# Kernel tuning notes

Measured on AMD Instinct MI355X. Metric: run time of the kernel, lower is better.

Reference implementation:

```python
import jax, jax.numpy as jnp
import numpy as np

USER = 1000
CATE = 1400
FEAT = 128
B = 8192


def setup_inputs() -> dict:
    key = jax.random.key(0)
    ks = jax.random.split(key, 16)
    s = 0.05
    return {
        "feat": jax.random.normal(ks[0], (B, FEAT), jnp.float32),
        "fcat": jax.random.randint(ks[1], (B, 3), 0, CATE),
        "fusr": jax.random.randint(ks[2], (B,), 0, USER),
        "fitm": jax.random.randint(ks[3], (B,), 0, USER),
        "flg": 1,
        "usr_w": jax.random.normal(ks[4], (USER, 128), jnp.float32) * s,
        "cate_w": jax.random.normal(ks[5], (CATE, 11), jnp.float32) * s,
        "cmat_w": jax.random.normal(ks[6], (CATE, 11 * 11), jnp.float32) * s,
        "cbias_w": jax.random.normal(ks[7], (CATE, 11), jnp.float32) * s,
        "ubias_w": jax.random.normal(ks[8], (USER, 128), jnp.float32) * s,
        "cbiasb_w": jax.random.normal(ks[9], (CATE, 95), jnp.float32) * s,
        "fc0_w": jax.random.normal(ks[10], (95, FEAT), jnp.float32) * s,
        "fc0_b": jax.random.normal(ks[11], (95,), jnp.float32) * s,
        "cvismat_w": jax.random.normal(ks[12], (CATE, 95 * 95), jnp.float32) * s,
        "cvisbias_w": jax.random.normal(ks[13], (CATE, 95), jnp.float32) * s,
    }


def reference(feat, fcat, fusr, fitm, flg, usr_w, cate_w, cmat_w, cbias_w,
              ubias_w, cbiasb_w, fc0_w, fc0_b, cvismat_w, cvisbias_w):
    b = feat.shape[0]
    c0, c1, c2 = fcat[:, 0], fcat[:, 1], fcat[:, 2]
    # cat1.repeat(1,11)*cmat .view(b,11,11).sum(2) == batched matvec M @ v
    cat1 = cate_w[c0]                                              # [b,11]
    cat2 = jnp.einsum('bij,bj->bi', cmat_w[c1].reshape(b, 11, 11), cat1) + cbias_w[c1]
    cat3 = jnp.einsum('bij,bj->bi', cmat_w[c2].reshape(b, 11, 11), cat2) + cbias_w[c2]
    cbias = jnp.concatenate([jnp.zeros((b, 33), feat.dtype), cbiasb_w[c2]], axis=1)  # [b,128]
    p0 = feat @ fc0_w.T + fc0_b                                    # [b,95]
    itmq = jnp.einsum('bij,bj->bi', cvismat_w[c2].reshape(b, 95, 95), p0) + cvisbias_w[c2]
    pitm = jnp.concatenate([cat1, cat2, cat3, itmq], axis=1)       # [b,128]
    if flg == 0:
        return jnp.sum((pitm + ubias_w[fusr]) * (usr_w[fusr] + cbias), axis=1).reshape(-1, 1)
    # flg != 0: score against all USER users; algebraic expansion avoids [b,USER,128]
    # sum_d (pitm[b,d]+ubias[u,d])*(usr[u,d]+cbias[b,d])
    return (pitm @ usr_w.T
            + jnp.sum(pitm * cbias, axis=1, keepdims=True)
            + jnp.sum(ubias_w * usr_w, axis=1)[None, :]
            + cbias @ ubias_w.T)                                    # [b,USER]
```

## Files before the change

### kernel.cpp

```cpp
#include <hip/hip_runtime.h>
#include <hip/hip_bf16.h>

typedef unsigned short u16;
typedef unsigned int u32;
typedef u16 u16x4 __attribute__((ext_vector_type(4)));
typedef u16 u16x8 __attribute__((ext_vector_type(8)));
typedef __bf16 bf16x8 __attribute__((ext_vector_type(8)));
typedef float f32x4 __attribute__((ext_vector_type(4)));

#define USER_N 1000
#define CATE_N 1400
#define FEAT_N 128
#define B_N 8192
#define CAP 64

__device__ __forceinline__ float b2f(u16 u) {
    union { u32 i; float f; } v; v.i = ((u32)u) << 16; return v.f;
}
__device__ __forceinline__ u16 f2b(float f) {
    union { float f; u32 i; } v; v.f = f;
    u32 x = v.i;
    u32 r = (x + 0x7fffu + ((x >> 16) & 1u)) >> 16;
    return (u16)r;
}
__device__ __forceinline__ f32x4 ld4u(const float* p) {
    f32x4 v; __builtin_memcpy(&v, p, 16); return v;
}
__device__ __forceinline__ bf16x8 cvt8(f32x4 a, f32x4 b) {
    u16x8 r = {f2b(a.x), f2b(a.y), f2b(a.z), f2b(a.w),
               f2b(b.x), f2b(b.y), f2b(b.z), f2b(b.w)};
    return __builtin_bit_cast(bf16x8, r);
}
__device__ __forceinline__ size_t xa_addr(int b, int k) {
    return (size_t)(b >> 4) * 4096 + (size_t)(k >> 3) * 128 + (b & 15) * 8 + (k & 7);
}

__global__ __launch_bounds__(256) void pack_kernel(
    const float* __restrict__ usr_w, const float* __restrict__ ubias_w,
    const float* __restrict__ feat, const float* __restrict__ fc0_w,
    u16* __restrict__ WB, float* __restrict__ t, int* __restrict__ counts,
    u16* __restrict__ FA, u16* __restrict__ WF)
{
    const int bx = blockIdx.x;
    const int tid = threadIdx.x;
    if (bx < 128) {
        if (bx == 0) {
            for (int i = tid; i < CATE_N; i += 256) counts[i] = 0;
        }
        const int gid = bx * 256 + tid;
        const int u = gid >> 5;
        const int l = gid & 31;
        float part = 0.f;
        u16x4 wa = {0, 0, 0, 0}, wb = {0, 0, 0, 0};
        if (u < USER_N) {
            f32x4 a4 = *(const f32x4*)&usr_w[u * 128 + l * 4];
            f32x4 b4 = *(const f32x4*)&ubias_w[u * 128 + l * 4];
            wa = (u16x4){f2b(a4.x), f2b(a4.y), f2b(a4.z), f2b(a4.w)};
            wb = (u16x4){f2b(b4.x), f2b(b4.y), f2b(b4.z), f2b(b4.w)};
            part = a4.x * b4.x + a4.y * b4.y + a4.z * b4.z + a4.w * b4.w;
        }
        const int nb = u >> 4, lm = u & 15;
        const int ks = l >> 3, quad = (l >> 1) & 3, j0 = (l & 1) * 4;
        *(u16x4*)&WB[(size_t)(nb * 8 + ks) * 512 + quad * 128 + lm * 8 + j0] = wa;
        *(u16x4*)&WB[(size_t)(nb * 8 + 4 + ks) * 512 + quad * 128 + lm * 8 + j0] = wb;
        part += __shfl_xor(part, 16, 32);
        part += __shfl_xor(part, 8, 32);
        part += __shfl_xor(part, 4, 32);
        part += __shfl_xor(part, 2, 32);
        part += __shfl_xor(part, 1, 32);
        if (l == 0) t[u] = part;
    } else if (bx < 256) {
        const int lm = tid >> 4;
        const int q4 = tid & 15;
        const int ks = q4 >> 2, quad = q4 & 3;
        #pragma unroll
        for (int it = 0; it < 4; ++it) {
            const int mt = (bx - 128) * 4 + it;
            const float* fr = feat + (size_t)(mt * 16 + lm) * 128 + ks * 32 + quad * 8;
            f32x4 lo = *(const f32x4*)fr;
            f32x4 hi = *(const f32x4*)(fr + 4);
            *(u16x8*)&FA[(size_t)mt * 2048 + ks * 512 + quad * 128 + lm * 8] =
                __builtin_bit_cast(u16x8, cvt8(lo, hi));
        }
    } else {
        const int lm = tid & 15;
        const int quad = (tid >> 4) & 3;
        const int ks = tid >> 6;
        #pragma unroll
        for (int nt = 0; nt < 6; ++nt) {
            const int i = nt * 16 + lm;
            const bool v = (i < 95);
            f32x4 lo = {0, 0, 0, 0}, hi = {0, 0, 0, 0};
            if (v) {
                const float* br = fc0_w + (size_t)i * 128 + ks * 32 + quad * 8;
                lo = *(const f32x4*)br;
                hi = *(const f32x4*)(br + 4);
            }
            *(u16x8*)&WF[(size_t)(nt * 4 + ks) * 512 + quad * 128 + lm * 8] =
                __builtin_bit_cast(u16x8, cvt8(lo, hi));
        }
    }
}

__global__ __launch_bounds__(256) void p0chain_kernel(
    const int* __restrict__ fcat,
    const float* __restrict__ cate_w, const float* __restrict__ cmat_w,
    const float* __restrict__ cbias_w, const float* __restrict__ fc0_b,
    const u16* __restrict__ FA, const u16* __restrict__ WF,
    int* __restrict__ counts, int* __restrict__ bins,
    u16* __restrict__ p0Gb, u16* __restrict__ XA)
{
    const int tid = threadIdx.x;
    const int w = tid >> 6, lane = tid & 63;
    const int lm = lane & 15, quad = lane >> 4;
    const int b0 = blockIdx.x * 32;

    if (tid < 32) {
        int row = b0 + tid;
        int c2v = fcat[row * 3 + 2];
        int slot = atomicAdd(&counts[c2v], 1);
        if (slot < CAP) bins[c2v * CAP + slot] = row;
    }

    const int mt = blockIdx.x * 2 + (w >> 1);
    const int nth = w & 1;
    bf16x8 a[4];
    const u16* fa = FA + (size_t)mt * 2048 + quad * 128 + lm * 8;
    #pragma unroll
    for (int ks = 0; ks < 4; ++ks)
        a[ks] = __builtin_bit_cast(bf16x8, *(const u16x8*)(fa + ks * 512));

    #pragma unroll
    for (int nt3 = 0; nt3 < 3; ++nt3) {
        const int nt = nth * 3 + nt3;
        const u16* wf = WF + (size_t)(nt * 4) * 512 + quad * 128 + lm * 8;
        f32x4 acc = {0.f, 0.f, 0.f, 0.f};
        #pragma unroll
        for (int ks = 0; ks < 4; ++ks)
            acc = __builtin_amdgcn_mfma_f32_16x16x32_bf16(
                a[ks], __builtin_bit_cast(bf16x8, *(const u16x8*)(wf + ks * 512)),
                acc, 0, 0, 0);
        const int i = nt * 16 + lm;
        const bool v = (i < 95);
        const float bias = v ? fc0_b[i] : 0.f;
        #pragma unroll
        for (int r = 0; r < 4; ++r) {
            int row = mt * 16 + quad * 4 + r;
            p0Gb[(size_t)row * 96 + i] = v ? f2b(acc[r] + bias) : (u16)0;
        }
    }

    __shared__ float chS[4][8][34];
    const int r8 = lane & 7, oct = lane >> 3;
    const int row = b0 + w * 8 + r8;
    const int c0 = fcat[row * 3 + 0];
    const int c1 = fcat[row * 3 + 1];
    const int c2 = fcat[row * 3 + 2];

    #pragma unroll
    for (int dd = 0; dd < 2; ++dd) {
        int d = oct + dd * 8;
        if (d < 11) chS[w][r8][d] = cate_w[c0 * 11 + d];
    }
    asm volatile("s_waitcnt lgkmcnt(0)" ::: "memory");
    __builtin_amdgcn_sched_barrier(0);

    float st[2];
    #pragma unroll
    for (int dd = 0; dd < 2; ++dd) {
        int d = oct + dd * 8;
        st[dd] = 0.f;
        if (d < 11) {
            float acc = cbias_w[c1 * 11 + d];
            const float* cm = cmat_w + (size_t)c1 * 121 + d * 11;
            #pragma unroll
            for (int j = 0; j < 11; ++j) acc += cm[j] * chS[w][r8][j];
            st[dd] = acc;
        }
    }
    #pragma unroll
    for (int dd = 0; dd < 2; ++dd) {
        int d = oct + dd * 8;
        if (d < 11) chS[w][r8][11 + d] = st[dd];
    }
    asm volatile("s_waitcnt lgkmcnt(0)" ::: "memory");
    __builtin_amdgcn_sched_barrier(0);

    #pragma unroll
    for (int dd = 0; dd < 2; ++dd) {
        int d = oct + dd * 8;
        st[dd] = 0.f;
        if (d < 11) {
            float acc = cbias_w[c2 * 11 + d];
            const float* cm = cmat_w + (size_t)c2 * 121 + d * 11;
            #pragma unroll
            for (int j = 0; j < 11; ++j) acc += cm[j] * chS[w][r8][11 + j];
            st[dd] = acc;
        }
    }
    #pragma unroll
    for (int dd = 0; dd < 2; ++dd) {
        int d = oct + dd * 8;
        if (d < 11) chS[w][r8][22 + d] = st[dd];
    }
    asm volatile("s_waitcnt lgkmcnt(0)" ::: "memory");
    __builtin_amdgcn_sched_barrier(0);

    for (int idx = lane; idx < 8 * 33; idx += 64) {
        int r2 = idx / 33, cc = idx - r2 * 33;
        int bb = b0 + w * 8 + r2;
        XA[xa_addr(bb, cc)] = f2b(chS[w][r2][cc]);
        XA[xa_addr(bb, 128 + cc)] = 0;
    }
}

__global__ __launch_bounds__(128) void itmq_kernel(
    const float* __restrict__ cvismat_w, const float* __restrict__ cvisbias_w,
    const float* __restrict__ cbiasb_w,
    const int* __restrict__ counts, const int* __restrict__ bins,
    const u16* __restrict__ p0Gb,
    u16* __restrict__ XA, float* __restrict__ s_out)
{
    const int c = blockIdx.x;
    int n = counts[c];
    if (n <= 0) return;
    if (n > CAP) n = CAP;
    const int tid = threadIdx.x;
    const int wave = tid >> 6, lane = tid & 63;
    const int lm = lane & 15, quad = lane >> 4;

    __shared__ float qS[16 * 96];
    __shared__ float cvbS[96], cbbS[96];
    __shared__ u16   cbb16S[96];
    __shared__ int   brS[16];

    if (tid < 96) cvbS[tid] = (tid < 95) ? cvisbias_w[c * 95 + tid] : 0.f;
    if (tid >= 32) {
        int k = tid - 32;
        float v = (k < 95) ? cbiasb_w[c * 95 + k] : 0.f;
        cbbS[k] = v;
        cbb16S[k] = f2b(v);
    }

    bf16x8 bfr[3][3];
    #pragma unroll
    for (int tnt = 0; tnt < 3; ++tnt) {
        const int i = (wave * 3 + tnt) * 16 + lm;
        const bool v = (i < 95);
        const float* br = cvismat_w + (size_t)c * 9025 + (size_t)(v ? i : 0) * 95;
        #pragma unroll
        for (int ks = 0; ks < 3; ++ks) {
            f32x4 lo = {0,0,0,0}, hi = {0,0,0,0};
            if (v) {
                if (ks < 2 || quad < 3) {
                    lo = ld4u(br + ks * 32 + quad * 8);
                    hi = ld4u(br + ks * 32 + quad * 8 + 4);
                } else {
                    lo = ld4u(br + 88);
                    hi.x = br[92]; hi.y = br[93]; hi.z = br[94]; hi.w = 0.f;
                }
            }
            bfr[tnt][ks] = cvt8(lo, hi);
        }
    }

    for (int m0 = 0; m0 < n; m0 += 16) {
        const int am = m0 + lm;
        const int ab = bins[c * CAP + (am < n ? am : 0)];
        const u16* pr = p0Gb + (size_t)ab * 96 + quad * 8;
        bf16x8 a[3];
        #pragma unroll
        for (int ks = 0; ks < 3; ++ks)
            a[ks] = __builtin_bit_cast(bf16x8, *(const u16x8*)(pr + ks * 32));
        f32x4 acc[3] = {{0,0,0,0}, {0,0,0,0}, {0,0,0,0}};
        #pragma unroll
        for (int tnt = 0; tnt < 3; ++tnt)
            #pragma unroll
            for (int ks = 0; ks < 3; ++ks)
                acc[tnt] = __builtin_amdgcn_mfma_f32_16x16x32_bf16(
                    a[ks], bfr[tnt][ks], acc[tnt], 0, 0, 0);

        __syncthreads();
        if (tid < 16) brS[tid] = bins[c * CAP + ((m0 + tid < n) ? m0 + tid : 0)];
        #pragma unroll
        for (int tnt = 0; tnt < 3; ++tnt) {
            const int i = (wave * 3 + tnt) * 16 + lm;
            #pragma unroll
            for (int r = 0; r < 4; ++r)
                qS[(quad * 4 + r) * 96 + i] = acc[tnt][r] + cvbS[i];
        }
        __syncthreads();

        {
            const int rr = tid >> 3, q8 = tid & 7;
            float p = 0.f;
            if (m0 + rr < n)
                for (int i = q8; i < 95; i += 8) p += qS[rr * 96 + i] * cbbS[i];
            p += __shfl_xor(p, 4, 8);
            p += __shfl_xor(p, 2, 8);
            p += __shfl_xor(p, 1, 8);
            if (q8 == 0 && m0 + rr < n) s_out[brS[rr]] = p;
        }
        const int nv = min(16, n - m0);
        for (int idx = tid; idx < nv * 95; idx += 128) {
            int r2 = idx / 95;
            int col = idx - r2 * 95;
            int bb = brS[r2];
            XA[xa_addr(bb, 33 + col)] = f2b(qS[r2 * 96 + col]);
            XA[xa_addr(bb, 161 + col)] = cbb16S[col];
        }
    }
}

__global__ __launch_bounds__(256) void gemm_kernel(
    const u16* __restrict__ XA, const u16* __restrict__ WB,
    const float* __restrict__ s, const float* __restrict__ t,
    float* __restrict__ out)
{
    const int tid = threadIdx.x;
    const int wave = tid >> 6;
    const int lane = tid & 63;
    const int lm = lane & 15;
    const int quad = lane >> 4;
    const int lofs = quad * 128 + lm * 8;

    const int bid = blockIdx.x;
    const int g = bid & 7;
    const int p = bid >> 3;
    const int mb = p * 4 + wave;
    const u16* abase = XA + (size_t)mb * 4096 + lofs;
    const u16* bbase = WB + (size_t)(g * 8) * 4096 + lofs;

    f32x4 acc[8];
    #pragma unroll
    for (int j = 0; j < 8; ++j) acc[j] = (f32x4){0.f, 0.f, 0.f, 0.f};

    #pragma unroll 2
    for (int ks = 0; ks < 8; ++ks) {
        const int o = ks * 512;
        bf16x8 a = __builtin_bit_cast(bf16x8, *(const u16x8*)(abase + o));
        #pragma unroll
        for (int j = 0; j < 8; ++j) {
            bf16x8 b = __builtin_bit_cast(bf16x8,
                *(const u16x8*)(bbase + (size_t)j * 4096 + o));
            acc[j] = __builtin_amdgcn_mfma_f32_16x16x32_bf16(a, b, acc[j], 0, 0, 0);
        }
    }

    const int m0 = mb * 16;
    float sv[4];
    #pragma unroll
    for (int r = 0; r < 4; ++r) sv[r] = s[m0 + quad * 4 + r];

    #pragma unroll
    for (int j = 0; j < 8; ++j) {
        int u = g * 128 + j * 16 + lm;
        if (u < USER_N) {
            float tv = t[u];
            #pragma unroll
            for (int r = 0; r < 4; ++r) {
                int ob = m0 + quad * 4 + r;
                out[(size_t)ob * USER_N + u] = acc[j][r] + sv[r] + tv;
            }
        }
    }
}

extern "C" void kernel_launch(void* const* d_in, const int* in_sizes, int n_in,
                              void* d_out, int out_size, void* d_ws, size_t ws_size,
                              hipStream_t stream) {
    const float* feat      = (const float*)d_in[0];
    const int*   fcat      = (const int*)d_in[1];
    const float* usr_w     = (const float*)d_in[5];
    const float* cate_w    = (const float*)d_in[6];
    const float* cmat_w    = (const float*)d_in[7];
    const float* cbias_w   = (const float*)d_in[8];
    const float* ubias_w   = (const float*)d_in[9];
    const float* cbiasb_w  = (const float*)d_in[10];
    const float* fc0_w     = (const float*)d_in[11];
    const float* fc0_b     = (const float*)d_in[12];
    const float* cvismat_w = (const float*)d_in[13];
    const float* cvisbias_w= (const float*)d_in[14];
    float* out = (float*)d_out;

    char* ws = (char*)d_ws;
    u16*   XA     = (u16*)(ws);
    u16*   WB     = (u16*)(ws + 4194304);
    float* s      = (float*)(ws + 4718592);
    float* t      = (float*)(ws + 4751360);
    int*   counts = (int*)(ws + 4755456);
    int*   bins   = (int*)(ws + 4761056);
    u16*   p0Gb   = (u16*)(ws + 5119456);
    u16*   FA     = (u16*)(ws + 6692320);
    u16*   WF     = (u16*)(ws + 8789472);

    pack_kernel<<<257, 256, 0, stream>>>(usr_w, ubias_w, feat, fc0_w,
                                         WB, t, counts, FA, WF);
    p0chain_kernel<<<256, 256, 0, stream>>>(fcat, cate_w, cmat_w, cbias_w,
                                            fc0_b, FA, WF, counts, bins,
                                            p0Gb, XA);
    itmq_kernel<<<CATE_N, 128, 0, stream>>>(cvismat_w, cvisbias_w, cbiasb_w,
                                            counts, bins, p0Gb, XA, s);
    gemm_kernel<<<1024, 256, 0, stream>>>(XA, WB, s, t, out);
}
```

Measured before the change: 161.4 us.

## Fuse pack and p0chain kernels, bin rows per category by scanning fcat

Merges the packing kernel into the p0/chain kernel. The feat and fc0_w tiles are now converted to bf16 in registers right before the MFMA, so the FA/WF staging buffers and one kernel launch go away. The global atomic binning (counts/bins) is replaced by each itmq block scanning all of fcat for its own category and building a row list in shared memory. This drops the counts reset and the inter-kernel dependency on bins. In exchange, each of the 1400 blocks reads the full 8192-entry fcat column, and fc0_w is reloaded and converted redundantly by every block.

```diff
diff --git a/kernel.cpp b/kernel.cpp
--- a/kernel.cpp
+++ b/kernel.cpp
@@ -35,19 +35,20 @@
     return (size_t)(b >> 4) * 4096 + (size_t)(k >> 3) * 128 + (b & 15) * 8 + (k & 7);
 }
 
-__global__ __launch_bounds__(256) void pack_kernel(
+__global__ __launch_bounds__(256) void prep_kernel(
+    const float* __restrict__ feat, const int* __restrict__ fcat,
+    const float* __restrict__ cate_w, const float* __restrict__ cmat_w,
+    const float* __restrict__ cbias_w, const float* __restrict__ fc0_w,
+    const float* __restrict__ fc0_b,
     const float* __restrict__ usr_w, const float* __restrict__ ubias_w,
-    const float* __restrict__ feat, const float* __restrict__ fc0_w,
-    u16* __restrict__ WB, float* __restrict__ t, int* __restrict__ counts,
-    u16* __restrict__ FA, u16* __restrict__ WF)
+    u16* __restrict__ WB, float* __restrict__ t,
+    u16* __restrict__ p0Gb, u16* __restrict__ XA)
 {
     const int bx = blockIdx.x;
     const int tid = threadIdx.x;
-    if (bx < 128) {
-        if (bx == 0) {
-            for (int i = tid; i < CATE_N; i += 256) counts[i] = 0;
-        }
-        const int gid = bx * 256 + tid;
+
+    if (bx >= 256) {
+        const int gid = (bx - 256) * 256 + tid;
         const int u = gid >> 5;
         const int l = gid & 31;
         float part = 0.f;
@@ -68,80 +69,38 @@
         part += __shfl_xor(part, 4, 32);
         part += __shfl_xor(part, 2, 32);
         part += __shfl_xor(part, 1, 32);
-        if (l == 0) t[u] = part;
-    } else if (bx < 256) {
-        const int lm = tid >> 4;
-        const int q4 = tid & 15;
-        const int ks = q4 >> 2, quad = q4 & 3;
-        #pragma unroll
-        for (int it = 0; it < 4; ++it) {
-            const int mt = (bx - 128) * 4 + it;
-            const float* fr = feat + (size_t)(mt * 16 + lm) * 128 + ks * 32 + quad * 8;
-            f32x4 lo = *(const f32x4*)fr;
-            f32x4 hi = *(const f32x4*)(fr + 4);
-            *(u16x8*)&FA[(size_t)mt * 2048 + ks * 512 + quad * 128 + lm * 8] =
-                __builtin_bit_cast(u16x8, cvt8(lo, hi));
-        }
-    } else {
-        const int lm = tid & 15;
-        const int quad = (tid >> 4) & 3;
-        const int ks = tid >> 6;
-        #pragma unroll
-        for (int nt = 0; nt < 6; ++nt) {
-            const int i = nt * 16 + lm;
-            const bool v = (i < 95);
-            f32x4 lo = {0, 0, 0, 0}, hi = {0, 0, 0, 0};
-            if (v) {
-                const float* br = fc0_w + (size_t)i * 128 + ks * 32 + quad * 8;
-                lo = *(const f32x4*)br;
-                hi = *(const f32x4*)(br + 4);
-            }
-            *(u16x8*)&WF[(size_t)(nt * 4 + ks) * 512 + quad * 128 + lm * 8] =
-                __builtin_bit_cast(u16x8, cvt8(lo, hi));
-        }
-    }
-}
-
-__global__ __launch_bounds__(256) void p0chain_kernel(
-    const int* __restrict__ fcat,
-    const float* __restrict__ cate_w, const float* __restrict__ cmat_w,
-    const float* __restrict__ cbias_w, const float* __restrict__ fc0_b,
-    const u16* __restrict__ FA, const u16* __restrict__ WF,
-    int* __restrict__ counts, int* __restrict__ bins,
-    u16* __restrict__ p0Gb, u16* __restrict__ XA)
-{
-    const int tid = threadIdx.x;
+        if (l == 0 && u < USER_N) t[u] = part;
+        return;
+    }
+
     const int w = tid >> 6, lane = tid & 63;
     const int lm = lane & 15, quad = lane >> 4;
-    const int b0 = blockIdx.x * 32;
-
-    if (tid < 32) {
-        int row = b0 + tid;
-        int c2v = fcat[row * 3 + 2];
-        int slot = atomicAdd(&counts[c2v], 1);
-        if (slot < CAP) bins[c2v * CAP + slot] = row;
-    }
-
-    const int mt = blockIdx.x * 2 + (w >> 1);
+    const int b0 = bx * 32;
+
+    const int mt = bx * 2 + (w >> 1);
     const int nth = w & 1;
     bf16x8 a[4];
-    const u16* fa = FA + (size_t)mt * 2048 + quad * 128 + lm * 8;
+    const float* frw = feat + (size_t)(mt * 16 + lm) * 128 + quad * 8;
     #pragma unroll
     for (int ks = 0; ks < 4; ++ks)
-        a[ks] = __builtin_bit_cast(bf16x8, *(const u16x8*)(fa + ks * 512));
+        a[ks] = cvt8(*(const f32x4*)(frw + ks * 32),
+                     *(const f32x4*)(frw + ks * 32 + 4));
 
     #pragma unroll
     for (int nt3 = 0; nt3 < 3; ++nt3) {
         const int nt = nth * 3 + nt3;
-        const u16* wf = WF + (size_t)(nt * 4) * 512 + quad * 128 + lm * 8;
-        f32x4 acc = {0.f, 0.f, 0.f, 0.f};
-        #pragma unroll
-        for (int ks = 0; ks < 4; ++ks)
-            acc = __builtin_amdgcn_mfma_f32_16x16x32_bf16(
-                a[ks], __builtin_bit_cast(bf16x8, *(const u16x8*)(wf + ks * 512)),
-                acc, 0, 0, 0);
         const int i = nt * 16 + lm;
         const bool v = (i < 95);
+        const float* br = fc0_w + (size_t)(v ? i : 0) * 128 + quad * 8;
+        f32x4 acc = {0.f, 0.f, 0.f, 0.f};
+        #pragma unroll
+        for (int ks = 0; ks < 4; ++ks) {
+            f32x4 lo = {0,0,0,0}, hi = {0,0,0,0};
+            if (v) { lo = *(const f32x4*)(br + ks * 32);
+                     hi = *(const f32x4*)(br + ks * 32 + 4); }
+            acc = __builtin_amdgcn_mfma_f32_16x16x32_bf16(a[ks], cvt8(lo, hi),
+                                                          acc, 0, 0, 0);
+        }
         const float bias = v ? fc0_b[i] : 0.f;
         #pragma unroll
         for (int r = 0; r < 4; ++r) {
@@ -216,15 +175,11 @@
 
 __global__ __launch_bounds__(128) void itmq_kernel(
     const float* __restrict__ cvismat_w, const float* __restrict__ cvisbias_w,
-    const float* __restrict__ cbiasb_w,
-    const int* __restrict__ counts, const int* __restrict__ bins,
+    const float* __restrict__ cbiasb_w, const int* __restrict__ fcat,
     const u16* __restrict__ p0Gb,
     u16* __restrict__ XA, float* __restrict__ s_out)
 {
     const int c = blockIdx.x;
-    int n = counts[c];
-    if (n <= 0) return;
-    if (n > CAP) n = CAP;
     const int tid = threadIdx.x;
     const int wave = tid >> 6, lane = tid & 63;
     const int lm = lane & 15, quad = lane >> 4;
@@ -232,8 +187,10 @@
     __shared__ float qS[16 * 96];
     __shared__ float cvbS[96], cbbS[96];
     __shared__ u16   cbb16S[96];
-    __shared__ int   brS[16];
-
+    __shared__ int   rlist[CAP];
+    __shared__ int   nS;
+
+    if (tid == 0) nS = 0;
     if (tid < 96) cvbS[tid] = (tid < 95) ? cvisbias_w[c * 95 + tid] : 0.f;
     if (tid >= 32) {
         int k = tid - 32;
@@ -242,7 +199,7 @@
         cbb16S[k] = f2b(v);
     }
 
-    bf16x8 bfr[3][3];
+    f32x4 rawL[3][3], rawH[3][3];
     #pragma unroll
     for (int tnt = 0; tnt < 3; ++tnt) {
         const int i = (wave * 3 + tnt) * 16 + lm;
@@ -260,13 +217,33 @@
                     hi.x = br[92]; hi.y = br[93]; hi.z = br[94]; hi.w = 0.f;
                 }
             }
-            bfr[tnt][ks] = cvt8(lo, hi);
-        }
-    }
+            rawL[tnt][ks] = lo; rawH[tnt][ks] = hi;
+        }
+    }
+
+    __syncthreads();
+    #pragma unroll 4
+    for (int it = 0; it < B_N / 128; ++it) {
+        int r = it * 128 + tid;
+        if (fcat[r * 3 + 2] == c) {
+            int sl = atomicAdd(&nS, 1);
+            if (sl < CAP) rlist[sl] = r;
+        }
+    }
+    __syncthreads();
+    int n = nS < CAP ? nS : CAP;
+    if (n <= 0) return;
+
+    bf16x8 bfr[3][3];
+    #pragma unroll
+    for (int tnt = 0; tnt < 3; ++tnt)
+        #pragma unroll
+        for (int ks = 0; ks < 3; ++ks)
+            bfr[tnt][ks] = cvt8(rawL[tnt][ks], rawH[tnt][ks]);
 
     for (int m0 = 0; m0 < n; m0 += 16) {
         const int am = m0 + lm;
-        const int ab = bins[c * CAP + (am < n ? am : 0)];
+        const int ab = rlist[am < n ? am : 0];
         const u16* pr = p0Gb + (size_t)ab * 96 + quad * 8;
         bf16x8 a[3];
         #pragma unroll
@@ -281,7 +258,6 @@
                     a[ks], bfr[tnt][ks], acc[tnt], 0, 0, 0);
 
         __syncthreads();
-        if (tid < 16) brS[tid] = bins[c * CAP + ((m0 + tid < n) ? m0 + tid : 0)];
         #pragma unroll
         for (int tnt = 0; tnt < 3; ++tnt) {
             const int i = (wave * 3 + tnt) * 16 + lm;
@@ -299,13 +275,13 @@
             p += __shfl_xor(p, 4, 8);
             p += __shfl_xor(p, 2, 8);
             p += __shfl_xor(p, 1, 8);
-            if (q8 == 0 && m0 + rr < n) s_out[brS[rr]] = p;
+            if (q8 == 0 && m0 + rr < n) s_out[rlist[m0 + rr]] = p;
         }
         const int nv = min(16, n - m0);
         for (int idx = tid; idx < nv * 95; idx += 128) {
             int r2 = idx / 95;
             int col = idx - r2 * 95;
-            int bb = brS[r2];
+            int bb = rlist[m0 + r2];
             XA[xa_addr(bb, 33 + col)] = f2b(qS[r2 * 96 + col]);
             XA[xa_addr(bb, 161 + col)] = cbb16S[col];
         }
@@ -388,18 +364,12 @@
     u16*   WB     = (u16*)(ws + 4194304);
     float* s      = (float*)(ws + 4718592);
     float* t      = (float*)(ws + 4751360);
-    int*   counts = (int*)(ws + 4755456);
-    int*   bins   = (int*)(ws + 4761056);
-    u16*   p0Gb   = (u16*)(ws + 5119456);
-    u16*   FA     = (u16*)(ws + 6692320);
-    u16*   WF     = (u16*)(ws + 8789472);
-
-    pack_kernel<<<257, 256, 0, stream>>>(usr_w, ubias_w, feat, fc0_w,
-                                         WB, t, counts, FA, WF);
-    p0chain_kernel<<<256, 256, 0, stream>>>(fcat, cate_w, cmat_w, cbias_w,
-                                            fc0_b, FA, WF, counts, bins,
-                                            p0Gb, XA);
+    u16*   p0Gb   = (u16*)(ws + 4755456);
+
+    prep_kernel<<<384, 256, 0, stream>>>(feat, fcat, cate_w, cmat_w, cbias_w,
+                                         fc0_w, fc0_b, usr_w, ubias_w,
+                                         WB, t, p0Gb, XA);
     itmq_kernel<<<CATE_N, 128, 0, stream>>>(cvismat_w, cvisbias_w, cbiasb_w,
-                                            counts, bins, p0Gb, XA, s);
+                                            fcat, p0Gb, XA, s);
     gemm_kernel<<<1024, 256, 0, stream>>>(XA, WB, s, t, out);
 }
```

Result: slower. 173.4 us (+7.4%).
